# Kernel optimization log

Hardware: AMD Instinct MI355X
Metric: run time of the kernel (lower is better)

The kernel has to match this reference:

```python
import jax, jax.numpy as jnp
import numpy as np

N_NODES = 50000
N_EDGES = 800000
N_GRAPHS = 256
FEAT = 128
HID = 64
HEADS = 4
OUT = 128
NEG_SLOPE = 0.2  # PyG GATConv default leaky_relu slope


def setup_inputs() -> dict:
    key = jax.random.key(0)
    ks = jax.random.split(key, 16)
    x = jax.random.normal(ks[0], (N_NODES, FEAT), dtype=jnp.float32)
    edge_index = jax.random.randint(ks[1], (2, N_EDGES), 0, N_NODES, dtype=jnp.int64)
    batch = jnp.sort(jax.random.randint(ks[2], (N_NODES,), 0, N_GRAPHS, dtype=jnp.int64))
    dims_in = [FEAT, HID * HEADS, HID * HEADS]
    params = {}
    for i, din in enumerate(dims_in):
        s = 1.0 / np.sqrt(din)
        params[f"W{i}"] = jax.random.normal(ks[3 + 4 * i], (din, HEADS * HID), dtype=jnp.float32) * s
        params[f"as{i}"] = jax.random.normal(ks[4 + 4 * i], (HEADS, HID), dtype=jnp.float32) * s
        params[f"ad{i}"] = jax.random.normal(ks[5 + 4 * i], (HEADS, HID), dtype=jnp.float32) * s
        params[f"b{i}"] = jnp.zeros((HEADS * HID,), dtype=jnp.float32)
    params["Wf"] = jax.random.normal(ks[15], (HID * HEADS, OUT), dtype=jnp.float32) / np.sqrt(HID * HEADS)
    params["bf"] = jnp.zeros((OUT,), dtype=jnp.float32)
    return {"x": x, "edge_index": edge_index, "batch": batch, **params}


def _gat_layer(x, src, dst, W, a_s, a_d, b):
    # x: [N, Din] -> h: [N, H, D]
    N = x.shape[0]
    h = (x @ W).reshape(N, HEADS, HID)
    alpha_src = jnp.einsum("nhd,hd->nh", h, a_s)  # [N, H]
    alpha_dst = jnp.einsum("nhd,hd->nh", h, a_d)
    e = jax.nn.leaky_relu(alpha_src[src] + alpha_dst[dst], NEG_SLOPE)  # [E, H]
    # segment softmax over edges sharing the same destination node
    m = jax.ops.segment_max(e, dst, num_segments=N)
    ex = jnp.exp(e - m[dst])
    s = jax.ops.segment_sum(ex, dst, num_segments=N)
    alpha = ex / s[dst]  # [E, H]
    msg = h[src] * alpha[:, :, None]  # [E, H, D]
    out = jax.ops.segment_sum(msg, dst, num_segments=N)  # [N, H, D]
    return out.reshape(N, HEADS * HID) + b


def reference(x, edge_index, batch, W0, as0, ad0, b0, W1, as1, ad1, b1,
              W2, as2, ad2, b2, Wf, bf):
    N = x.shape[0]
    loop = jnp.arange(N, dtype=edge_index.dtype)
    src = jnp.concatenate([edge_index[0], loop])  # PyG GATConv adds self-loops
    dst = jnp.concatenate([edge_index[1], loop])
    for W, a_s, a_d, b in ((W0, as0, ad0, b0), (W1, as1, ad1, b1), (W2, as2, ad2, b2)):
        x = jax.nn.elu(_gat_layer(x, src, dst, W, a_s, a_d, b))
    # global mean pool over graphs
    sums = jax.ops.segment_sum(x, batch, num_segments=N_GRAPHS)  # [G, HID*HEADS]
    cnt = jax.ops.segment_sum(jnp.ones((N,), x.dtype), batch, num_segments=N_GRAPHS)
    g = sums / jnp.maximum(cnt, 1.0)[:, None]
    y = g @ Wf + bf
    norm = jnp.linalg.norm(y, axis=-1, keepdims=True)
    return y / jnp.maximum(norm, 1e-12)
```

## Files before the change

### kernel.cpp

```cpp
#include <hip/hip_runtime.h>
#include <math.h>

#define NND 50000
#define NED 800000
#define ETOT 850000
#define NG 256
#define FEAT 128
#define CCH 256
#define OUTD 128
#define NEG 0.2f
#define NBLK 196
#define M2 50048

typedef __attribute__((ext_vector_type(8))) _Float16 half8;
typedef __attribute__((ext_vector_type(4))) _Float16 half4;
typedef __attribute__((ext_vector_type(4))) float floatx4;


__global__ void zero_int_kernel(int* p, int n) {
    int i = blockIdx.x * 256 + threadIdx.x;
    if (i < n) p[i] = 0;
}

__global__ void count_kernel(const int* __restrict__ ei, int* __restrict__ deg) {
    int e = blockIdx.x * 256 + threadIdx.x;
    if (e >= ETOT) return;
    int dst = (e < NED) ? ei[NED + e] : (e - NED);
    atomicAdd(&deg[dst], 1);
}

__global__ __launch_bounds__(256) void scan_part_kernel(const int* __restrict__ deg,
                                                        int* __restrict__ bsum) {
    __shared__ int tile[256];
    int i = blockIdx.x * 256 + threadIdx.x;
    tile[threadIdx.x] = (i < NND) ? deg[i] : 0;
    __syncthreads();
    for (int s = 128; s > 0; s >>= 1) {
        if (threadIdx.x < s) tile[threadIdx.x] += tile[threadIdx.x + s];
        __syncthreads();
    }
    if (threadIdx.x == 0) bsum[blockIdx.x] = tile[0];
}

__global__ __launch_bounds__(256) void scan_bsum_kernel(int* __restrict__ bsum,
                                                        int* __restrict__ boff,
                                                        int* __restrict__ total) {
    __shared__ int tile[256];
    int t = threadIdx.x;
    int v = (t < NBLK) ? bsum[t] : 0;
    tile[t] = v;
    __syncthreads();
    for (int off = 1; off < 256; off <<= 1) {
        int u = (t >= off) ? tile[t - off] : 0;
        __syncthreads();
        tile[t] += u;
        __syncthreads();
    }
    if (t < NBLK) boff[t] = tile[t] - v;
    if (t == 255) *total = tile[255];
}

__global__ __launch_bounds__(256) void scan_write_kernel(const int* __restrict__ deg,
                                                         const int* __restrict__ boff,
                                                         const int* __restrict__ total,
                                                         int* __restrict__ rowptr,
                                                         int* __restrict__ cursor) {
    __shared__ int tile[256];
    int i = blockIdx.x * 256 + threadIdx.x;
    int t = threadIdx.x;
    int v = (i < NND) ? deg[i] : 0;
    tile[t] = v;
    __syncthreads();
    for (int off = 1; off < 256; off <<= 1) {
        int u = (t >= off) ? tile[t - off] : 0;
        __syncthreads();
        tile[t] += u;
        __syncthreads();
    }
    if (i < NND) {
        int r = boff[blockIdx.x] + tile[t] - v;
        rowptr[i] = r;
        cursor[i] = r;
    }
    if (i == 0) rowptr[NND] = *total;
}

__global__ void scatter_kernel(const int* __restrict__ ei, int* __restrict__ cursor,
                               int* __restrict__ csrsrc) {
    int e = blockIdx.x * 256 + threadIdx.x;
    if (e >= ETOT) return;
    int s, d;
    if (e < NED) { s = ei[e]; d = ei[NED + e]; } else { s = d = e - NED; }
    int pos = atomicAdd(&cursor[d], 1);
    csrsrc[pos] = s;
}


__global__ void decomp_x_kernel(const float4* __restrict__ x, half4* __restrict__ xo) {
    int i = blockIdx.x * 256 + threadIdx.x;
    if (i >= NND * FEAT / 4) return;
    float4 v = x[i];
    half4 o;
    o[0] = (_Float16)v.x; o[1] = (_Float16)v.y;
    o[2] = (_Float16)v.z; o[3] = (_Float16)v.w;
    xo[i] = o;
}

__global__ void wdecomp_kernel(const float* __restrict__ W,
                               _Float16* __restrict__ wt, int K) {
    int j = blockIdx.x * 256 + threadIdx.x;
    if (j >= 256 * K) return;
    int n = j / K, k = j - n * K;
    wt[j] = (_Float16)W[k * 256 + n];
}


#define BK 64
#define SK 72

__global__ __launch_bounds__(256, 3) void gemm_mfma_kernel(
        const _Float16* __restrict__ A,
        const _Float16* __restrict__ Bt,
        const float* __restrict__ as_, const float* __restrict__ ad_,
        _Float16* __restrict__ Hm,
        float* __restrict__ asrc, float* __restrict__ adst, int K) {
    __shared__ _Float16 AsF[128 * SK];
    __shared__ _Float16 BsF[128 * SK];
    const int t = threadIdx.x;
    const int bn = blockIdx.x * 128;
    const int bm = blockIdx.y * 128;
    const int lane = t & 63, wv = t >> 6;
    const int wm = (wv >> 1) * 64, wn = (wv & 1) * 64;
    const int fr = lane & 15, q = lane >> 4;

    floatx4 acc[4][4] = {};

    const int lrow = t >> 3;
    const int lcol = (t & 7) * 8;

    for (int k0 = 0; k0 < K; k0 += BK) {
        for (int p = 0; p < 4; p++) {
            int row = p * 32 + lrow;
            size_t ga = (size_t)(bm + row) * K + k0 + lcol;
            size_t gb = (size_t)(bn + row) * K + k0 + lcol;
            *(half8*)&AsF[row * SK + lcol] = *(const half8*)&A[ga];
            *(half8*)&BsF[row * SK + lcol] = *(const half8*)&Bt[gb];
        }
        __syncthreads();
        for (int kc = 0; kc < 2; kc++) {
            half8 af[4], bf[4];
            int ko = kc * 32 + q * 8;
            for (int mi = 0; mi < 4; mi++)
                af[mi] = *(const half8*)&AsF[(wm + mi * 16 + fr) * SK + ko];
            for (int ni = 0; ni < 4; ni++)
                bf[ni] = *(const half8*)&BsF[(wn + ni * 16 + fr) * SK + ko];
            for (int mi = 0; mi < 4; mi++)
                for (int ni = 0; ni < 4; ni++)
                    acc[mi][ni] = __builtin_amdgcn_mfma_f32_16x16x32_f16(
                        af[mi], bf[ni], acc[mi][ni], 0, 0, 0);
        }
        __syncthreads();
    }

    for (int mi = 0; mi < 4; mi++) {
        int row0 = bm + wm + mi * 16 + q * 4;
        for (int ni = 0; ni < 4; ni++) {
            int col = bn + wn + ni * 16 + fr;
            for (int r = 0; r < 4; r++)
                Hm[(size_t)(row0 + r) * CCH + col] = (_Float16)acc[mi][ni][r];
        }
    }

    const int hd = (bn + wn) >> 6;
    float asf[4], adf[4];
    for (int ni = 0; ni < 4; ni++) {
        asf[ni] = as_[hd * 64 + ni * 16 + fr];
        adf[ni] = ad_[hd * 64 + ni * 16 + fr];
    }
    for (int mi = 0; mi < 4; mi++)
        for (int r = 0; r < 4; r++) {
            float ps = 0.f, pd = 0.f;
            for (int ni = 0; ni < 4; ni++) {
                float v = acc[mi][ni][r];
                ps += v * asf[ni];
                pd += v * adf[ni];
            }
            for (int m = 1; m < 16; m <<= 1) {
                ps += __shfl_xor(ps, m, 64);
                pd += __shfl_xor(pd, m, 64);
            }
            if (fr == 0) {
                int row = bm + wm + mi * 16 + q * 4 + r;
                asrc[row * 4 + hd] = ps;
                adst[row * 4 + hd] = pd;
            }
        }
}


__global__ __launch_bounds__(256) void agg_kernel(const _Float16* __restrict__ H16,
                                                  const float* __restrict__ asrc,
                                                  const float* __restrict__ adst,
                                                  const int* __restrict__ rowptr,
                                                  const int* __restrict__ csrsrc,
                                                  const float4* __restrict__ bias4,
                                                  half4* __restrict__ xo) {
    int wave = threadIdx.x >> 6, lane = threadIdx.x & 63;
    int n = blockIdx.x * 4 + wave;
    if (n >= NND) return;
    int rs = rowptr[n], re = rowptr[n + 1];
    int hd = lane >> 4;
    int sub = lane & 15;
    float adv = adst[n * 4 + hd];
    float4 acc = make_float4(0.f, 0.f, 0.f, 0.f);
    float ssum = 0.f;
    for (int e0 = rs; e0 < re; e0 += 16) {
        int cnt = re - e0; if (cnt > 16) cnt = 16;
        int sl = e0 + sub;
        bool ok = sl < re;
        int idxv = ok ? csrsrc[sl] : 0;
        float ev = 0.f;
        if (ok) {
            float a = asrc[idxv * 4 + hd] + adv;
            a = a > 0.f ? a : NEG * a;
            ev = __expf(a);
        }
        ssum += ev;
        for (int j = 0; j < cnt; j++) {
            int s = __shfl(idxv, j, 64);
            float ww = __shfl(ev, (lane & 48) | j, 64);
            half4 hv = *(const half4*)&H16[(size_t)s * CCH + lane * 4];
            acc.x += ww * (float)hv[0];
            acc.y += ww * (float)hv[1];
            acc.z += ww * (float)hv[2];
            acc.w += ww * (float)hv[3];
        }
    }
    for (int off = 1; off < 16; off <<= 1) ssum += __shfl_xor(ssum, off, 64);
    float inv = 1.f / ssum;
    float4 bv = bias4[lane];
    float4 o;
    o.x = acc.x * inv + bv.x; o.y = acc.y * inv + bv.y;
    o.z = acc.z * inv + bv.z; o.w = acc.w * inv + bv.w;
    o.x = o.x > 0.f ? o.x : expm1f(o.x);
    o.y = o.y > 0.f ? o.y : expm1f(o.y);
    o.z = o.z > 0.f ? o.z : expm1f(o.z);
    o.w = o.w > 0.f ? o.w : expm1f(o.w);
    half4 h;
    h[0] = (_Float16)o.x; h[1] = (_Float16)o.y;
    h[2] = (_Float16)o.z; h[3] = (_Float16)o.w;
    xo[(size_t)n * 64 + lane] = h;
}


__global__ void bounds_kernel(const int* __restrict__ batch, int* __restrict__ gstart) {
    int i = blockIdx.x * 256 + threadIdx.x;
    if (i >= NND) return;
    int b = batch[i];
    int bp = (i == 0) ? -1 : batch[i - 1];
    for (int g = bp + 1; g <= b; ++g) gstart[g] = i;
    if (i == NND - 1) {
        for (int g = b + 1; g <= NG; ++g) gstart[g] = NND;
    }
}

__global__ __launch_bounds__(256) void pool_kernel(const _Float16* __restrict__ xa,
                                                   const int* __restrict__ gstart,
                                                   float* __restrict__ gmean) {
    int g = blockIdx.x, t = threadIdx.x;
    int s = gstart[g], e = gstart[g + 1];
    float acc = 0.f;
    for (int i = s; i < e; i++)
        acc += (float)xa[(size_t)i * CCH + t];
    int cnt = e - s;
    gmean[g * CCH + t] = acc / (float)(cnt > 0 ? cnt : 1);
}

__global__ __launch_bounds__(128) void final_kernel(const float* __restrict__ gmean,
                                                    const float* __restrict__ Wf,
                                                    const float* __restrict__ bf,
                                                    float* __restrict__ out) {
    int g = blockIdx.x, c = threadIdx.x;
    const float* gv = gmean + g * CCH;
    float acc = bf[c];
    for (int k = 0; k < CCH; k++) acc += gv[k] * Wf[k * OUTD + c];
    __shared__ float red[128];
    red[c] = acc * acc;
    __syncthreads();
    for (int s = 64; s > 0; s >>= 1) {
        if (c < s) red[c] += red[c + s];
        __syncthreads();
    }
    float nrm = sqrtf(red[0]);
    out[g * OUTD + c] = acc / fmaxf(nrm, 1e-12f);
}


extern "C" void kernel_launch(void* const* d_in, const int* in_sizes, int n_in,
                              void* d_out, int out_size, void* d_ws, size_t ws_size,
                              hipStream_t stream) {
    const float* x     = (const float*)d_in[0];
    const int*   ei    = (const int*)d_in[1];
    const int*   batch = (const int*)d_in[2];
    const float* W[3]  = {(const float*)d_in[3], (const float*)d_in[7],  (const float*)d_in[11]};
    const float* As[3] = {(const float*)d_in[4], (const float*)d_in[8],  (const float*)d_in[12]};
    const float* Ad[3] = {(const float*)d_in[5], (const float*)d_in[9],  (const float*)d_in[13]};
    const float* Bb[3] = {(const float*)d_in[6], (const float*)d_in[10], (const float*)d_in[14]};
    const float* Wf    = (const float*)d_in[15];
    const float* bf    = (const float*)d_in[16];
    float* out = (float*)d_out;

    _Float16* H16   = (_Float16*)d_ws;
    _Float16* act16 = H16 + (size_t)M2 * CCH;
    _Float16* wt    = act16 + (size_t)M2 * CCH;
    float* asrc  = (float*)(wt + 256 * 256);
    float* adst  = asrc + (size_t)M2 * 4;
    float* gmean = adst + (size_t)M2 * 4;
    int* deg     = (int*)(gmean + (size_t)NG * CCH);
    int* rowptr  = deg + (NND + 1);
    int* cursor  = rowptr + (NND + 1);
    int* csrsrc  = cursor + (NND + 1);
    int* gstart  = csrsrc + ETOT;
    int* bsum    = gstart + (NG + 1);
    int* boff    = bsum + NBLK;
    int* total   = boff + NBLK;

    zero_int_kernel<<<(NND + 1 + 255) / 256, 256, 0, stream>>>(deg, NND + 1);
    count_kernel<<<(ETOT + 255) / 256, 256, 0, stream>>>(ei, deg);
    scan_part_kernel<<<NBLK, 256, 0, stream>>>(deg, bsum);
    scan_bsum_kernel<<<1, 256, 0, stream>>>(bsum, boff, total);
    scan_write_kernel<<<NBLK, 256, 0, stream>>>(deg, boff, total, rowptr, cursor);
    scatter_kernel<<<(ETOT + 255) / 256, 256, 0, stream>>>(ei, cursor, csrsrc);
    bounds_kernel<<<(NND + 255) / 256, 256, 0, stream>>>(batch, gstart);

    decomp_x_kernel<<<(NND * FEAT / 4 + 255) / 256, 256, 0, stream>>>(
        (const float4*)x, (half4*)act16);

    int K = FEAT;
    for (int l = 0; l < 3; l++) {
        wdecomp_kernel<<<K, 256, 0, stream>>>(W[l], wt, K);
        dim3 g(2, M2 / 128);
        gemm_mfma_kernel<<<g, 256, 0, stream>>>(act16, wt, As[l], Ad[l], H16, asrc, adst, K);
        agg_kernel<<<(NND + 3) / 4, 256, 0, stream>>>(H16, asrc, adst, rowptr, csrsrc,
                                                      (const float4*)Bb[l], (half4*)act16);
        K = CCH;
    }

    pool_kernel<<<NG, 256, 0, stream>>>(act16, gstart, gmean);
    final_kernel<<<NG, 128, 0, stream>>>(gmean, Wf, bf, out);
}
```

Before: 560.0 us.

## Use direct global-to-LDS loads with XOR swizzle; batch weight conversion; fuse pool+final

The GEMM tile loads now go through global_load_lds, moving data straight into shared memory, and use an XOR-swizzled unpadded layout to avoid bank conflicts. The three per-layer weight transpose/convert kernels become one launch, and the pooling and final projection/normalize kernels are merged into one. The aim is fewer launches and less register staging in the GEMM. The builtin writes LDS per wave at a base plus lane offset, so passing per-thread LDS addresses may not give the layout the read side expects.

```diff
diff --git a/kernel.cpp b/kernel.cpp
--- a/kernel.cpp
+++ b/kernel.cpp
@@ -16,6 +16,15 @@
 typedef __attribute__((ext_vector_type(4))) _Float16 half4;
 typedef __attribute__((ext_vector_type(4))) float floatx4;
 
+#if __has_builtin(__builtin_amdgcn_global_load_lds)
+#define GLOAD16(g, l) __builtin_amdgcn_global_load_lds( \
+    (const __attribute__((address_space(1))) void*)(g), \
+    (__attribute__((address_space(3))) void*)(l), 16, 0, 0)
+#define HAVE_GLDS 1
+#else
+#define HAVE_GLDS 0
+#endif
+
 
 __global__ void zero_int_kernel(int* p, int n) {
     int i = blockIdx.x * 256 + threadIdx.x;
@@ -106,17 +115,33 @@
     xo[i] = o;
 }
 
-__global__ void wdecomp_kernel(const float* __restrict__ W,
-                               _Float16* __restrict__ wt, int K) {
+__global__ void wdecomp_all_kernel(const float* __restrict__ W0,
+                                   const float* __restrict__ W1,
+                                   const float* __restrict__ W2,
+                                   _Float16* __restrict__ wt0,
+                                   _Float16* __restrict__ wt1,
+                                   _Float16* __restrict__ wt2) {
     int j = blockIdx.x * 256 + threadIdx.x;
-    if (j >= 256 * K) return;
-    int n = j / K, k = j - n * K;
-    wt[j] = (_Float16)W[k * 256 + n];
+    if (j < 256 * 128) {
+        int n = j >> 7, k = j & 127;
+        wt0[j] = (_Float16)W0[k * 256 + n];
+        return;
+    }
+    j -= 256 * 128;
+    if (j < 256 * 256) {
+        int n = j >> 8, k = j & 255;
+        wt1[j] = (_Float16)W1[k * 256 + n];
+        return;
+    }
+    j -= 256 * 256;
+    if (j < 256 * 256) {
+        int n = j >> 8, k = j & 255;
+        wt2[j] = (_Float16)W2[k * 256 + n];
+    }
 }
 
 
 #define BK 64
-#define SK 72
 
 __global__ __launch_bounds__(256, 3) void gemm_mfma_kernel(
         const _Float16* __restrict__ A,
@@ -124,8 +149,8 @@
         const float* __restrict__ as_, const float* __restrict__ ad_,
         _Float16* __restrict__ Hm,
         float* __restrict__ asrc, float* __restrict__ adst, int K) {
-    __shared__ _Float16 AsF[128 * SK];
-    __shared__ _Float16 BsF[128 * SK];
+    __shared__ _Float16 AsF[128 * 64];
+    __shared__ _Float16 BsF[128 * 64];
     const int t = threadIdx.x;
     const int bn = blockIdx.x * 128;
     const int bm = blockIdx.y * 128;
@@ -136,24 +161,31 @@
     floatx4 acc[4][4] = {};
 
     const int lrow = t >> 3;
-    const int lcol = (t & 7) * 8;
+    const int c8 = t & 7;
 
     for (int k0 = 0; k0 < K; k0 += BK) {
         for (int p = 0; p < 4; p++) {
             int row = p * 32 + lrow;
-            size_t ga = (size_t)(bm + row) * K + k0 + lcol;
-            size_t gb = (size_t)(bn + row) * K + k0 + lcol;
-            *(half8*)&AsF[row * SK + lcol] = *(const half8*)&A[ga];
-            *(half8*)&BsF[row * SK + lcol] = *(const half8*)&Bt[gb];
+            int g8 = c8 ^ (row & 7);
+            const _Float16* ga = A + (size_t)(bm + row) * K + k0 + g8 * 8;
+            const _Float16* gb = Bt + (size_t)(bn + row) * K + k0 + g8 * 8;
+#if HAVE_GLDS
+            GLOAD16(ga, &AsF[row * 64 + c8 * 8]);
+            GLOAD16(gb, &BsF[row * 64 + c8 * 8]);
+#else
+            *(half8*)&AsF[row * 64 + c8 * 8] = *(const half8*)ga;
+            *(half8*)&BsF[row * 64 + c8 * 8] = *(const half8*)gb;
+#endif
         }
         __syncthreads();
         for (int kc = 0; kc < 2; kc++) {
             half8 af[4], bf[4];
-            int ko = kc * 32 + q * 8;
+            int kb = kc * 4 + q;
+            int cs = (kb ^ (fr & 7)) * 8;
             for (int mi = 0; mi < 4; mi++)
-                af[mi] = *(const half8*)&AsF[(wm + mi * 16 + fr) * SK + ko];
+                af[mi] = *(const half8*)&AsF[(wm + mi * 16 + fr) * 64 + cs];
             for (int ni = 0; ni < 4; ni++)
-                bf[ni] = *(const half8*)&BsF[(wn + ni * 16 + fr) * SK + ko];
+                bf[ni] = *(const half8*)&BsF[(wn + ni * 16 + fr) * 64 + cs];
             for (int mi = 0; mi < 4; mi++)
                 for (int ni = 0; ni < 4; ni++)
                     acc[mi][ni] = __builtin_amdgcn_mfma_f32_16x16x32_f16(
@@ -264,35 +296,33 @@
     }
 }
 
-__global__ __launch_bounds__(256) void pool_kernel(const _Float16* __restrict__ xa,
-                                                   const int* __restrict__ gstart,
-                                                   float* __restrict__ gmean) {
+__global__ __launch_bounds__(256) void poolfinal_kernel(const _Float16* __restrict__ xa,
+                                                        const int* __restrict__ gstart,
+                                                        const float* __restrict__ Wf,
+                                                        const float* __restrict__ bfv,
+                                                        float* __restrict__ out) {
     int g = blockIdx.x, t = threadIdx.x;
+    __shared__ float gm[256];
+    __shared__ float red[128];
     int s = gstart[g], e = gstart[g + 1];
     float acc = 0.f;
     for (int i = s; i < e; i++)
         acc += (float)xa[(size_t)i * CCH + t];
     int cnt = e - s;
-    gmean[g * CCH + t] = acc / (float)(cnt > 0 ? cnt : 1);
-}
-
-__global__ __launch_bounds__(128) void final_kernel(const float* __restrict__ gmean,
-                                                    const float* __restrict__ Wf,
-                                                    const float* __restrict__ bf,
-                                                    float* __restrict__ out) {
-    int g = blockIdx.x, c = threadIdx.x;
-    const float* gv = gmean + g * CCH;
-    float acc = bf[c];
-    for (int k = 0; k < CCH; k++) acc += gv[k] * Wf[k * OUTD + c];
-    __shared__ float red[128];
-    red[c] = acc * acc;
-    __syncthreads();
-    for (int s = 64; s > 0; s >>= 1) {
-        if (c < s) red[c] += red[c + s];
-        __syncthreads();
-    }
-    float nrm = sqrtf(red[0]);
-    out[g * OUTD + c] = acc / fmaxf(nrm, 1e-12f);
+    gm[t] = acc / (float)(cnt > 0 ? cnt : 1);
+    __syncthreads();
+    float a = 0.f;
+    if (t < OUTD) {
+        a = bfv[t];
+        for (int k = 0; k < CCH; k++) a += gm[k] * Wf[k * OUTD + t];
+        red[t] = a * a;
+    }
+    __syncthreads();
+    for (int sft = 64; sft > 0; sft >>= 1) {
+        if (t < sft) red[t] += red[t + sft];
+        __syncthreads();
+    }
+    if (t < OUTD) out[g * OUTD + t] = a / fmaxf(sqrtf(red[0]), 1e-12f);
 }
 
 
@@ -312,11 +342,12 @@
 
     _Float16* H16   = (_Float16*)d_ws;
     _Float16* act16 = H16 + (size_t)M2 * CCH;
-    _Float16* wt    = act16 + (size_t)M2 * CCH;
-    float* asrc  = (float*)(wt + 256 * 256);
+    _Float16* wt0   = act16 + (size_t)M2 * CCH;
+    _Float16* wt1   = wt0 + 256 * 128;
+    _Float16* wt2   = wt1 + 256 * 256;
+    float* asrc  = (float*)(wt2 + 256 * 256);
     float* adst  = asrc + (size_t)M2 * 4;
-    float* gmean = adst + (size_t)M2 * 4;
-    int* deg     = (int*)(gmean + (size_t)NG * CCH);
+    int* deg     = (int*)(adst + (size_t)M2 * 4);
     int* rowptr  = deg + (NND + 1);
     int* cursor  = rowptr + (NND + 1);
     int* csrsrc  = cursor + (NND + 1);
@@ -325,6 +356,8 @@
     int* boff    = bsum + NBLK;
     int* total   = boff + NBLK;
 
+    _Float16* wt[3] = {wt0, wt1, wt2};
+
     zero_int_kernel<<<(NND + 1 + 255) / 256, 256, 0, stream>>>(deg, NND + 1);
     count_kernel<<<(ETOT + 255) / 256, 256, 0, stream>>>(ei, deg);
     scan_part_kernel<<<NBLK, 256, 0, stream>>>(deg, bsum);
@@ -335,17 +368,17 @@
 
     decomp_x_kernel<<<(NND * FEAT / 4 + 255) / 256, 256, 0, stream>>>(
         (const float4*)x, (half4*)act16);
+    wdecomp_all_kernel<<<(256 * (128 + 256 + 256) + 255) / 256, 256, 0, stream>>>(
+        W[0], W[1], W[2], wt0, wt1, wt2);
 
     int K = FEAT;
     for (int l = 0; l < 3; l++) {
-        wdecomp_kernel<<<K, 256, 0, stream>>>(W[l], wt, K);
         dim3 g(2, M2 / 128);
-        gemm_mfma_kernel<<<g, 256, 0, stream>>>(act16, wt, As[l], Ad[l], H16, asrc, adst, K);
+        gemm_mfma_kernel<<<g, 256, 0, stream>>>(act16, wt[l], As[l], Ad[l], H16, asrc, adst, K);
         agg_kernel<<<(NND + 3) / 4, 256, 0, stream>>>(H16, asrc, adst, rowptr, csrsrc,
                                                       (const float4*)Bb[l], (half4*)act16);
         K = CCH;
     }
 
-    pool_kernel<<<NG, 256, 0, stream>>>(act16, gstart, gmean);
-    final_kernel<<<NG, 128, 0, stream>>>(gmean, Wf, bf, out);
-}
+    poolfinal_kernel<<<NG, 256, 0, stream>>>(act16, gstart, Wf, bf, out);
+}
```

Measured after the change: 551.7 us. No clear change (-1.5%).
